# Kernel tuning notes

Hardware: AMD Instinct MI355X
Metric: run time of the kernel (lower is better)

The kernel has to match this reference:

```python
import jax, jax.numpy as jnp
import numpy as np

S, B, H = 512, 32, 1024      # seq, batch, hidden_size
L = 4096                      # total spans (flattened ragged labels)
D = 1024                      # label_size (feature dim)
V = 32000                     # vocab size


def setup_inputs() -> dict:
    key = jax.random.key(0)
    ks = jax.random.split(key, 10)
    hidden = jax.random.normal(ks[0], (S, B, H), dtype=jnp.float32)
    span_bid = jax.random.randint(ks[1], (L,), 0, B)
    span_begin = jax.random.randint(ks[2], (L,), 0, S)
    span_end_m1 = jax.random.randint(ks[3], (L,), 0, S)  # (end - 1) index
    tags = jax.random.randint(ks[4], (L,), 0, V)
    # hidden2feature: Linear(2H -> D) with bias, Tanh
    W1 = jax.random.normal(ks[5], (D, 2 * H), dtype=jnp.float32) * (1.0 / np.sqrt(2 * H))
    b1 = jnp.zeros((D,), dtype=jnp.float32)
    # SoftmaxLoss h2o: Linear(D -> V, bias=False)
    Wout = jax.random.normal(ks[6], (V, D), dtype=jnp.float32) * (1.0 / np.sqrt(D))
    # discard probs from synthetic frequency counts
    counts = jax.random.uniform(ks[7], (V,), minval=1e-5, maxval=1.0)
    freqs = counts / counts.sum()
    discard_probs = jnp.clip(1.0 - jnp.sqrt(1e-4 / freqs), 0.0, None)
    return {"hidden": hidden, "W1": W1, "b1": b1, "Wout": Wout,
            "discard_probs": discard_probs, "span_bid": span_bid,
            "span_begin": span_begin, "span_end_m1": span_end_m1, "tags": tags}


def reference(hidden, W1, b1, Wout, discard_probs, span_bid, span_begin, span_end_m1, tags):
    # gather span endpoint embeddings: [L, H] each
    emb_b = hidden[span_begin, span_bid]
    emb_e = hidden[span_end_m1, span_bid]
    span_emb = jnp.concatenate([emb_b, emb_e], axis=-1)          # [L, 2H]
    feat = jnp.tanh(span_emb @ W1.T + b1)                        # [L, D]
    logits = feat @ Wout.T                                       # [L, V]
    logp = jax.nn.log_softmax(logits, axis=-1)
    nll = -jnp.take_along_axis(logp, tags[:, None], axis=-1)[:, 0]  # [L]
    scaled = 1.0 - discard_probs[tags]
    n_tags = tags.shape[0]
    return jnp.sum(nll * scaled) / (n_tags + 1e-5)
```

## Files before the change

kernel.cpp:

```cpp
#include <hip/hip_runtime.h>
#include <hip/hip_bf16.h>

#define LSPANS 4096
#define BB 32
#define HH 1024
#define DD 1024
#define VV 32000
#define K1 2048
#define NT2 250

typedef unsigned short u16;
typedef __attribute__((ext_vector_type(8))) short bf16x8v;
typedef __attribute__((ext_vector_type(4))) float f32x4v;

__device__ __forceinline__ u16 f2bf(float x) {
  union { float f; unsigned u; } v; v.f = x;
  unsigned r = (v.u >> 16) & 1u;
  return (u16)((v.u + 0x7fffu + r) >> 16);
}

__global__ void cvt_kernel(const float* __restrict__ in, u16* __restrict__ out, int n4) {
  int i = blockIdx.x * blockDim.x + threadIdx.x;
  int stride = gridDim.x * blockDim.x;
  for (; i < n4; i += stride) {
    float4 v = ((const float4*)in)[i];
    ushort4 o;
    o.x = f2bf(v.x); o.y = f2bf(v.y); o.z = f2bf(v.z); o.w = f2bf(v.w);
    ((ushort4*)out)[i] = o;
  }
}

__global__ void gather_kernel(const float* __restrict__ hidden,
                              const int* __restrict__ bid,
                              const int* __restrict__ sb,
                              const int* __restrict__ se,
                              u16* __restrict__ out) {
  int l = blockIdx.x;
  int t = threadIdx.x;
  int b  = bid[l];
  const float* p0 = hidden + ((size_t)sb[l] * BB + b) * HH;
  const float* p1 = hidden + ((size_t)se[l] * BB + b) * HH;
  u16* dst = out + (size_t)l * K1;
  float4 v0 = ((const float4*)p0)[t];
  float4 v1 = ((const float4*)p1)[t];
  ushort4 o0; o0.x = f2bf(v0.x); o0.y = f2bf(v0.y); o0.z = f2bf(v0.z); o0.w = f2bf(v0.w);
  ushort4 o1; o1.x = f2bf(v1.x); o1.y = f2bf(v1.y); o1.z = f2bf(v1.z); o1.w = f2bf(v1.w);
  ((ushort4*)dst)[t]          = o0;
  ((ushort4*)(dst + HH))[t]   = o1;
}

template <int K_, int EPI>
__launch_bounds__(256, 2)
__global__ void gemm_kernel(const u16* __restrict__ A, const u16* __restrict__ B,
                            int Ntot,
                            const float* __restrict__ bias, u16* __restrict__ feat_out,
                            const int* __restrict__ tags,
                            float* __restrict__ pmax, float* __restrict__ psum,
                            float* __restrict__ ltag) {
  __shared__ __align__(16) u16 As[128 * 64];
  __shared__ __align__(16) u16 Bs[128 * 64];
  __shared__ float rmax[2][128];
  __shared__ float rsum[2][128];
  __shared__ int   stags[128];

  const int tid  = threadIdx.x;
  const int lane = tid & 63;
  const int w    = tid >> 6;
  const int wm   = w & 1;
  const int wn   = w >> 1;
  const int q    = lane >> 4;
  const int lm   = lane & 15;
  const int mBase = blockIdx.x * 128;
  const int nBase = blockIdx.y * 128;

  if (EPI == 2 && tid < 128) stags[tid] = tags[mBase + tid];

  f32x4v acc[4][4];
#pragma unroll
  for (int i = 0; i < 4; ++i)
#pragma unroll
    for (int j = 0; j < 4; ++j) acc[i][j] = (f32x4v){0.f, 0.f, 0.f, 0.f};

  const int srow = w * 32 + (lane >> 3);
  const int scol = ((lane & 7) ^ (lane >> 3)) * 8;
  const u16* Ag = A + (size_t)(mBase + srow) * K_ + scol;
  const u16* Bg = B + (size_t)(nBase + srow) * K_ + scol;

  for (int k0 = 0; k0 < K_; k0 += 64) {
#pragma unroll
    for (int c = 0; c < 4; ++c) {
      __builtin_amdgcn_global_load_lds(
          (const __attribute__((address_space(1))) void*)(Ag + k0 + (size_t)c * 8 * K_),
          (__attribute__((address_space(3))) void*)(As + (w * 32 + c * 8) * 64), 16, 0, 0);
    }
#pragma unroll
    for (int c = 0; c < 4; ++c) {
      __builtin_amdgcn_global_load_lds(
          (const __attribute__((address_space(1))) void*)(Bg + k0 + (size_t)c * 8 * K_),
          (__attribute__((address_space(3))) void*)(Bs + (w * 32 + c * 8) * 64), 16, 0, 0);
    }
    __syncthreads();
#pragma unroll
    for (int kk = 0; kk < 64; kk += 32) {
      bf16x8v af[4], bfr[4];
      const int sw = lm & 7;
#pragma unroll
      for (int i = 0; i < 4; ++i) {
        int row = wm * 64 + i * 16 + lm;
        int kch = (kk >> 3) + q;
        af[i] = *(const bf16x8v*)(As + row * 64 + ((kch ^ sw) << 3));
      }
#pragma unroll
      for (int j = 0; j < 4; ++j) {
        int row = wn * 64 + j * 16 + lm;
        int kch = (kk >> 3) + q;
        bfr[j] = *(const bf16x8v*)(Bs + row * 64 + ((kch ^ sw) << 3));
      }
#pragma unroll
      for (int i = 0; i < 4; ++i)
#pragma unroll
        for (int j = 0; j < 4; ++j)
          acc[i][j] = __builtin_amdgcn_mfma_f32_16x16x32_bf16(af[i], bfr[j], acc[i][j], 0, 0, 0);
    }
    __syncthreads();
  }

  if constexpr (EPI == 1) {
    float bj[4];
#pragma unroll
    for (int j = 0; j < 4; ++j) bj[j] = bias[nBase + wn * 64 + j * 16 + lm];
#pragma unroll
    for (int i = 0; i < 4; ++i)
#pragma unroll
      for (int j = 0; j < 4; ++j)
#pragma unroll
        for (int r = 0; r < 4; ++r) {
          int tr = wm * 64 + i * 16 + q * 4 + r;
          int tc = wn * 64 + j * 16 + lm;
          float v = tanhf(acc[i][j][r] + bj[j]);
          feat_out[(size_t)(mBase + tr) * Ntot + nBase + tc] = f2bf(v);
        }
  }

  if constexpr (EPI == 2) {
#pragma unroll
    for (int i = 0; i < 4; ++i)
#pragma unroll
      for (int r = 0; r < 4; ++r) {
        float m = fmaxf(fmaxf(acc[i][0][r], acc[i][1][r]),
                        fmaxf(acc[i][2][r], acc[i][3][r]));
#pragma unroll
        for (int off = 1; off < 16; off <<= 1) m = fmaxf(m, __shfl_xor(m, off, 64));
        if (lm == 0) rmax[wn][wm * 64 + i * 16 + q * 4 + r] = m;
      }
    __syncthreads();
#pragma unroll
    for (int i = 0; i < 4; ++i)
#pragma unroll
      for (int r = 0; r < 4; ++r) {
        int tr = wm * 64 + i * 16 + q * 4 + r;
        float M = fmaxf(rmax[0][tr], rmax[1][tr]);
        float s = __expf(acc[i][0][r] - M) + __expf(acc[i][1][r] - M) +
                  __expf(acc[i][2][r] - M) + __expf(acc[i][3][r] - M);
#pragma unroll
        for (int off = 1; off < 16; off <<= 1) s += __shfl_xor(s, off, 64);
        if (lm == 0) rsum[wn][tr] = s;
      }
    __syncthreads();
    if (tid < 128) {
      float M = fmaxf(rmax[0][tid], rmax[1][tid]);
      float S = rsum[0][tid] + rsum[1][tid];
      pmax[(size_t)blockIdx.y * LSPANS + mBase + tid] = M;
      psum[(size_t)blockIdx.y * LSPANS + mBase + tid] = S;
    }
#pragma unroll
    for (int i = 0; i < 4; ++i)
#pragma unroll
      for (int r = 0; r < 4; ++r) {
        int tr = wm * 64 + i * 16 + q * 4 + r;
        int tg = stags[tr];
#pragma unroll
        for (int j = 0; j < 4; ++j) {
          int gc = nBase + wn * 64 + j * 16 + lm;
          if (tg == gc) ltag[mBase + tr] = acc[i][j][r];
        }
      }
  }
}

__launch_bounds__(256, 2)
__global__ void gemm1n64_kernel(const u16* __restrict__ A, const u16* __restrict__ B,
                                const float* __restrict__ bias,
                                u16* __restrict__ feat_out) {
  __shared__ __align__(16) u16 As[128 * 64];
  __shared__ __align__(16) u16 Bs[64 * 64];

  const int tid  = threadIdx.x;
  const int lane = tid & 63;
  const int w    = tid >> 6;
  const int wm   = w & 1;
  const int wn   = w >> 1;
  const int q    = lane >> 4;
  const int lm   = lane & 15;
  const int mBase = blockIdx.x * 128;
  const int nBase = blockIdx.y * 64;

  f32x4v acc[4][2];
#pragma unroll
  for (int i = 0; i < 4; ++i)
#pragma unroll
    for (int j = 0; j < 2; ++j) acc[i][j] = (f32x4v){0.f, 0.f, 0.f, 0.f};

  const int srowA = w * 32 + (lane >> 3);
  const int srowB = w * 16 + (lane >> 3);
  const int scol  = ((lane & 7) ^ (lane >> 3)) * 8;
  const u16* Ag = A + (size_t)(mBase + srowA) * K1 + scol;
  const u16* Bg = B + (size_t)(nBase + srowB) * K1 + scol;

  for (int k0 = 0; k0 < K1; k0 += 64) {
#pragma unroll
    for (int c = 0; c < 4; ++c) {
      __builtin_amdgcn_global_load_lds(
          (const __attribute__((address_space(1))) void*)(Ag + k0 + (size_t)c * 8 * K1),
          (__attribute__((address_space(3))) void*)(As + (w * 32 + c * 8) * 64), 16, 0, 0);
    }
#pragma unroll
    for (int c = 0; c < 2; ++c) {
      __builtin_amdgcn_global_load_lds(
          (const __attribute__((address_space(1))) void*)(Bg + k0 + (size_t)c * 8 * K1),
          (__attribute__((address_space(3))) void*)(Bs + (w * 16 + c * 8) * 64), 16, 0, 0);
    }
    __syncthreads();
#pragma unroll
    for (int kk = 0; kk < 64; kk += 32) {
      bf16x8v af[4], bfr[2];
      const int sw = lm & 7;
#pragma unroll
      for (int i = 0; i < 4; ++i) {
        int row = wm * 64 + i * 16 + lm;
        int kch = (kk >> 3) + q;
        af[i] = *(const bf16x8v*)(As + row * 64 + ((kch ^ sw) << 3));
      }
#pragma unroll
      for (int j = 0; j < 2; ++j) {
        int row = wn * 32 + j * 16 + lm;
        int kch = (kk >> 3) + q;
        bfr[j] = *(const bf16x8v*)(Bs + row * 64 + ((kch ^ sw) << 3));
      }
#pragma unroll
      for (int i = 0; i < 4; ++i)
#pragma unroll
        for (int j = 0; j < 2; ++j)
          acc[i][j] = __builtin_amdgcn_mfma_f32_16x16x32_bf16(af[i], bfr[j], acc[i][j], 0, 0, 0);
    }
    __syncthreads();
  }

  float bj[2];
#pragma unroll
  for (int j = 0; j < 2; ++j) bj[j] = bias[nBase + wn * 32 + j * 16 + lm];
#pragma unroll
  for (int i = 0; i < 4; ++i)
#pragma unroll
    for (int j = 0; j < 2; ++j)
#pragma unroll
      for (int r = 0; r < 4; ++r) {
        int tr = wm * 64 + i * 16 + q * 4 + r;
        int tc = wn * 32 + j * 16 + lm;
        float v = tanhf(acc[i][j][r] + bj[j]);
        feat_out[(size_t)(mBase + tr) * DD + nBase + tc] = f2bf(v);
      }
}

__global__ void finalize_kernel(const float* __restrict__ pmax, const float* __restrict__ psum,
                                const float* __restrict__ ltag, const int* __restrict__ tags,
                                const float* __restrict__ dprob, float* __restrict__ out) {
  const int lane = threadIdx.x & 63;
  const int wv   = threadIdx.x >> 6;
  const int row  = blockIdx.x * 4 + wv;

  float pmv[4], psv[4];
#pragma unroll
  for (int it = 0; it < 4; ++it) {
    int t = lane + it * 64;
    bool ok = t < NT2;
    pmv[it] = ok ? pmax[(size_t)t * LSPANS + row] : -1e30f;
    psv[it] = ok ? psum[(size_t)t * LSPANS + row] : 0.f;
  }
  float M = fmaxf(fmaxf(pmv[0], pmv[1]), fmaxf(pmv[2], pmv[3]));
#pragma unroll
  for (int off = 1; off < 64; off <<= 1) M = fmaxf(M, __shfl_xor(M, off, 64));
  float s = 0.f;
#pragma unroll
  for (int it = 0; it < 4; ++it) s += psv[it] * __expf(pmv[it] - M);
#pragma unroll
  for (int off = 1; off < 64; off <<= 1) s += __shfl_xor(s, off, 64);

  __shared__ float red[4];
  if (lane == 0) {
    float nll = M + logf(s) - ltag[row];
    float wgt = 1.0f - dprob[tags[row]];
    red[wv] = nll * wgt * (1.0f / (4096.0f + 1e-5f));
  }
  __syncthreads();
  if (threadIdx.x == 0) atomicAdd(out, red[0] + red[1] + red[2] + red[3]);
}

extern "C" void kernel_launch(void* const* d_in, const int* in_sizes, int n_in,
                              void* d_out, int out_size, void* d_ws, size_t ws_size,
                              hipStream_t stream) {
  const float* hidden = (const float*)d_in[0];
  const float* W1     = (const float*)d_in[1];
  const float* b1     = (const float*)d_in[2];
  const float* Wout   = (const float*)d_in[3];
  const float* dprob  = (const float*)d_in[4];
  const int*   bid    = (const int*)d_in[5];
  const int*   sb     = (const int*)d_in[6];
  const int*   se     = (const int*)d_in[7];
  const int*   tags   = (const int*)d_in[8];
  float* out = (float*)d_out;

  char* ws = (char*)d_ws;
  u16* A1    = (u16*)ws;                 ws += (size_t)LSPANS * K1 * 2;
  u16* W1b   = (u16*)ws;                 ws += (size_t)DD * K1 * 2;
  u16* Woutb = (u16*)ws;                 ws += (size_t)VV * DD * 2;
  u16* feat  = (u16*)ws;                 ws += (size_t)LSPANS * DD * 2;
  float* pmax = (float*)ws;              ws += (size_t)NT2 * LSPANS * 4;
  float* psum = (float*)ws;              ws += (size_t)NT2 * LSPANS * 4;
  float* ltag = (float*)ws;              ws += (size_t)LSPANS * 4;

  hipMemsetAsync(d_out, 0, sizeof(float), stream);

  {
    int n4 = DD * K1 / 4;
    cvt_kernel<<<(n4 + 255) / 256, 256, 0, stream>>>(W1, W1b, n4);
  }
  {
    int n4 = VV * DD / 4;
    cvt_kernel<<<(n4 + 255) / 256, 256, 0, stream>>>(Wout, Woutb, n4);
  }
  gather_kernel<<<LSPANS, 256, 0, stream>>>(hidden, bid, sb, se, A1);

  gemm1n64_kernel<<<dim3(LSPANS / 128, DD / 64), 256, 0, stream>>>(
      A1, W1b, b1, feat);

  gemm_kernel<DD, 2><<<dim3(LSPANS / 128, NT2), 256, 0, stream>>>(
      feat, Woutb, VV, nullptr, nullptr, tags, pmax, psum, ltag);

  finalize_kernel<<<LSPANS / 4, 256, 0, stream>>>(pmax, psum, ltag, tags, dprob, out);
}
```

Before: 587.2 us.

## Merge prep kernels and overlap Wout conversion with first GEMM, remap gemm2 tiles

Folds the hidden gather and the W1 conversion into one launch. The Wout fp32-to-bf16 conversion now runs as extra blocks inside the first GEMM launch, so that memory-bound work can overlap with the compute-bound GEMM and launch overhead drops. The second GEMM remaps block indices so consecutive blocks spread across N tiles, which changes L2 reuse of Wout and feat. The cost is more complex heterogeneous blocks, and the conversion blocks may compete with GEMM blocks for CU slots.

After: 611.9 us. +4.2%, slower.

```diff
diff --git a/kernel.cpp b/kernel.cpp
--- a/kernel.cpp
+++ b/kernel.cpp
@@ -19,44 +19,143 @@
   return (u16)((v.u + 0x7fffu + r) >> 16);
 }
 
-__global__ void cvt_kernel(const float* __restrict__ in, u16* __restrict__ out, int n4) {
-  int i = blockIdx.x * blockDim.x + threadIdx.x;
-  int stride = gridDim.x * blockDim.x;
-  for (; i < n4; i += stride) {
-    float4 v = ((const float4*)in)[i];
-    ushort4 o;
-    o.x = f2bf(v.x); o.y = f2bf(v.y); o.z = f2bf(v.z); o.w = f2bf(v.w);
-    ((ushort4*)out)[i] = o;
-  }
-}
-
-__global__ void gather_kernel(const float* __restrict__ hidden,
-                              const int* __restrict__ bid,
-                              const int* __restrict__ sb,
-                              const int* __restrict__ se,
-                              u16* __restrict__ out) {
-  int l = blockIdx.x;
-  int t = threadIdx.x;
-  int b  = bid[l];
-  const float* p0 = hidden + ((size_t)sb[l] * BB + b) * HH;
-  const float* p1 = hidden + ((size_t)se[l] * BB + b) * HH;
-  u16* dst = out + (size_t)l * K1;
-  float4 v0 = ((const float4*)p0)[t];
-  float4 v1 = ((const float4*)p1)[t];
-  ushort4 o0; o0.x = f2bf(v0.x); o0.y = f2bf(v0.y); o0.z = f2bf(v0.z); o0.w = f2bf(v0.w);
-  ushort4 o1; o1.x = f2bf(v1.x); o1.y = f2bf(v1.y); o1.z = f2bf(v1.z); o1.w = f2bf(v1.w);
-  ((ushort4*)dst)[t]          = o0;
-  ((ushort4*)(dst + HH))[t]   = o1;
-}
-
-template <int K_, int EPI>
+__global__ void prep1_kernel(const float* __restrict__ hidden,
+                             const int* __restrict__ bid,
+                             const int* __restrict__ sb,
+                             const int* __restrict__ se,
+                             u16* __restrict__ A1,
+                             const float* __restrict__ W1,
+                             u16* __restrict__ W1b) {
+  const int blk = blockIdx.x;
+  if (blk < LSPANS) {
+    const int l = blk;
+    const int t = threadIdx.x;
+    const int b = bid[l];
+    const float* p0 = hidden + ((size_t)sb[l] * BB + b) * HH;
+    const float* p1 = hidden + ((size_t)se[l] * BB + b) * HH;
+    u16* dst = A1 + (size_t)l * K1;
+    float4 v0 = ((const float4*)p0)[t];
+    float4 v1 = ((const float4*)p1)[t];
+    ushort4 o0; o0.x = f2bf(v0.x); o0.y = f2bf(v0.y); o0.z = f2bf(v0.z); o0.w = f2bf(v0.w);
+    ushort4 o1; o1.x = f2bf(v1.x); o1.y = f2bf(v1.y); o1.z = f2bf(v1.z); o1.w = f2bf(v1.w);
+    ((ushort4*)dst)[t]          = o0;
+    ((ushort4*)(dst + HH))[t]   = o1;
+  } else {
+    const int n4 = DD * K1 / 4;
+    int i = (blk - LSPANS) * 256 + threadIdx.x;
+    const int stride = 512 * 256;
+    for (; i < n4; i += stride) {
+      float4 v = ((const float4*)W1)[i];
+      ushort4 o;
+      o.x = f2bf(v.x); o.y = f2bf(v.y); o.z = f2bf(v.z); o.w = f2bf(v.w);
+      ((ushort4*)W1b)[i] = o;
+    }
+  }
+}
+
 __launch_bounds__(256, 2)
-__global__ void gemm_kernel(const u16* __restrict__ A, const u16* __restrict__ B,
-                            int Ntot,
-                            const float* __restrict__ bias, u16* __restrict__ feat_out,
-                            const int* __restrict__ tags,
-                            float* __restrict__ pmax, float* __restrict__ psum,
-                            float* __restrict__ ltag) {
+__global__ void prep2_kernel(const u16* __restrict__ A, const u16* __restrict__ B,
+                             const float* __restrict__ bias,
+                             u16* __restrict__ feat_out,
+                             const float* __restrict__ Wout,
+                             u16* __restrict__ Woutb) {
+  __shared__ __align__(16) u16 As[128 * 64];
+  __shared__ __align__(16) u16 Bs[64 * 64];
+
+  if (blockIdx.x < 512) {
+    const int tid  = threadIdx.x;
+    const int lane = tid & 63;
+    const int w    = tid >> 6;
+    const int wm   = w & 1;
+    const int wn   = w >> 1;
+    const int q    = lane >> 4;
+    const int lm   = lane & 15;
+    const int mBase = (blockIdx.x & 31) * 128;
+    const int nBase = (blockIdx.x >> 5) * 64;
+
+    f32x4v acc[4][2];
+#pragma unroll
+    for (int i = 0; i < 4; ++i)
+#pragma unroll
+      for (int j = 0; j < 2; ++j) acc[i][j] = (f32x4v){0.f, 0.f, 0.f, 0.f};
+
+    const int srowA = w * 32 + (lane >> 3);
+    const int srowB = w * 16 + (lane >> 3);
+    const int scol  = ((lane & 7) ^ (lane >> 3)) * 8;
+    const u16* Ag = A + (size_t)(mBase + srowA) * K1 + scol;
+    const u16* Bg = B + (size_t)(nBase + srowB) * K1 + scol;
+
+    for (int k0 = 0; k0 < K1; k0 += 64) {
+#pragma unroll
+      for (int c = 0; c < 4; ++c) {
+        __builtin_amdgcn_global_load_lds(
+            (const __attribute__((address_space(1))) void*)(Ag + k0 + (size_t)c * 8 * K1),
+            (__attribute__((address_space(3))) void*)(As + (w * 32 + c * 8) * 64), 16, 0, 0);
+      }
+#pragma unroll
+      for (int c = 0; c < 2; ++c) {
+        __builtin_amdgcn_global_load_lds(
+            (const __attribute__((address_space(1))) void*)(Bg + k0 + (size_t)c * 8 * K1),
+            (__attribute__((address_space(3))) void*)(Bs + (w * 16 + c * 8) * 64), 16, 0, 0);
+      }
+      __syncthreads();
+#pragma unroll
+      for (int kk = 0; kk < 64; kk += 32) {
+        bf16x8v af[4], bfr[2];
+        const int sw = lm & 7;
+#pragma unroll
+        for (int i = 0; i < 4; ++i) {
+          int row = wm * 64 + i * 16 + lm;
+          int kch = (kk >> 3) + q;
+          af[i] = *(const bf16x8v*)(As + row * 64 + ((kch ^ sw) << 3));
+        }
+#pragma unroll
+        for (int j = 0; j < 2; ++j) {
+          int row = wn * 32 + j * 16 + lm;
+          int kch = (kk >> 3) + q;
+          bfr[j] = *(const bf16x8v*)(Bs + row * 64 + ((kch ^ sw) << 3));
+        }
+#pragma unroll
+        for (int i = 0; i < 4; ++i)
+#pragma unroll
+          for (int j = 0; j < 2; ++j)
+            acc[i][j] = __builtin_amdgcn_mfma_f32_16x16x32_bf16(af[i], bfr[j], acc[i][j], 0, 0, 0);
+      }
+      __syncthreads();
+    }
+
+    float bj[2];
+#pragma unroll
+    for (int j = 0; j < 2; ++j) bj[j] = bias[nBase + wn * 32 + j * 16 + lm];
+#pragma unroll
+    for (int i = 0; i < 4; ++i)
+#pragma unroll
+      for (int j = 0; j < 2; ++j)
+#pragma unroll
+        for (int r = 0; r < 4; ++r) {
+          int tr = wm * 64 + i * 16 + q * 4 + r;
+          int tc = wn * 32 + j * 16 + lm;
+          float v = tanhf(acc[i][j][r] + bj[j]);
+          feat_out[(size_t)(mBase + tr) * DD + nBase + tc] = f2bf(v);
+        }
+  } else {
+    const int n4 = VV * DD / 4;
+    int i = (blockIdx.x - 512) * 256 + threadIdx.x;
+    const int stride = 2048 * 256;
+    for (; i < n4; i += stride) {
+      float4 v = ((const float4*)Wout)[i];
+      ushort4 o;
+      o.x = f2bf(v.x); o.y = f2bf(v.y); o.z = f2bf(v.z); o.w = f2bf(v.w);
+      ((ushort4*)Woutb)[i] = o;
+    }
+  }
+}
+
+__launch_bounds__(256, 2)
+__global__ void gemm2_kernel(const u16* __restrict__ A, const u16* __restrict__ B,
+                             const int* __restrict__ tags,
+                             float* __restrict__ pmax, float* __restrict__ psum,
+                             float* __restrict__ ltag) {
   __shared__ __align__(16) u16 As[128 * 64];
   __shared__ __align__(16) u16 Bs[128 * 64];
   __shared__ float rmax[2][128];
@@ -70,10 +169,14 @@
   const int wn   = w >> 1;
   const int q    = lane >> 4;
   const int lm   = lane & 15;
-  const int mBase = blockIdx.x * 128;
-  const int nBase = blockIdx.y * 128;
-
-  if (EPI == 2 && tid < 128) stags[tid] = tags[mBase + tid];
+  const int lin = blockIdx.y * 32 + blockIdx.x;
+  const int nl  = (lin & 7) * 1000 + (lin >> 3);
+  const int bx  = nl & 31;
+  const int by  = nl >> 5;
+  const int mBase = bx * 128;
+  const int nBase = by * 128;
+
+  if (tid < 128) stags[tid] = tags[mBase + tid];
 
   f32x4v acc[4][4];
 #pragma unroll
@@ -83,20 +186,20 @@
 
   const int srow = w * 32 + (lane >> 3);
   const int scol = ((lane & 7) ^ (lane >> 3)) * 8;
-  const u16* Ag = A + (size_t)(mBase + srow) * K_ + scol;
-  const u16* Bg = B + (size_t)(nBase + srow) * K_ + scol;
-
-  for (int k0 = 0; k0 < K_; k0 += 64) {
+  const u16* Ag = A + (size_t)(mBase + srow) * DD + scol;
+  const u16* Bg = B + (size_t)(nBase + srow) * DD + scol;
+
+  for (int k0 = 0; k0 < DD; k0 += 64) {
 #pragma unroll
     for (int c = 0; c < 4; ++c) {
       __builtin_amdgcn_global_load_lds(
-          (const __attribute__((address_space(1))) void*)(Ag + k0 + (size_t)c * 8 * K_),
+          (const __attribute__((address_space(1))) void*)(Ag + k0 + (size_t)c * 8 * DD),
           (__attribute__((address_space(3))) void*)(As + (w * 32 + c * 8) * 64), 16, 0, 0);
     }
 #pragma unroll
     for (int c = 0; c < 4; ++c) {
       __builtin_amdgcn_global_load_lds(
-          (const __attribute__((address_space(1))) void*)(Bg + k0 + (size_t)c * 8 * K_),
+          (const __attribute__((address_space(1))) void*)(Bg + k0 + (size_t)c * 8 * DD),
           (__attribute__((address_space(3))) void*)(Bs + (w * 32 + c * 8) * 64), 16, 0, 0);
     }
     __syncthreads();
@@ -125,151 +228,48 @@
     __syncthreads();
   }
 
-  if constexpr (EPI == 1) {
-    float bj[4];
-#pragma unroll
-    for (int j = 0; j < 4; ++j) bj[j] = bias[nBase + wn * 64 + j * 16 + lm];
-#pragma unroll
-    for (int i = 0; i < 4; ++i)
-#pragma unroll
-      for (int j = 0; j < 4; ++j)
-#pragma unroll
-        for (int r = 0; r < 4; ++r) {
-          int tr = wm * 64 + i * 16 + q * 4 + r;
-          int tc = wn * 64 + j * 16 + lm;
-          float v = tanhf(acc[i][j][r] + bj[j]);
-          feat_out[(size_t)(mBase + tr) * Ntot + nBase + tc] = f2bf(v);
-        }
-  }
-
-  if constexpr (EPI == 2) {
-#pragma unroll
-    for (int i = 0; i < 4; ++i)
-#pragma unroll
-      for (int r = 0; r < 4; ++r) {
-        float m = fmaxf(fmaxf(acc[i][0][r], acc[i][1][r]),
-                        fmaxf(acc[i][2][r], acc[i][3][r]));
-#pragma unroll
-        for (int off = 1; off < 16; off <<= 1) m = fmaxf(m, __shfl_xor(m, off, 64));
-        if (lm == 0) rmax[wn][wm * 64 + i * 16 + q * 4 + r] = m;
-      }
-    __syncthreads();
-#pragma unroll
-    for (int i = 0; i < 4; ++i)
-#pragma unroll
-      for (int r = 0; r < 4; ++r) {
-        int tr = wm * 64 + i * 16 + q * 4 + r;
-        float M = fmaxf(rmax[0][tr], rmax[1][tr]);
-        float s = __expf(acc[i][0][r] - M) + __expf(acc[i][1][r] - M) +
-                  __expf(acc[i][2][r] - M) + __expf(acc[i][3][r] - M);
-#pragma unroll
-        for (int off = 1; off < 16; off <<= 1) s += __shfl_xor(s, off, 64);
-        if (lm == 0) rsum[wn][tr] = s;
-      }
-    __syncthreads();
-    if (tid < 128) {
-      float M = fmaxf(rmax[0][tid], rmax[1][tid]);
-      float S = rsum[0][tid] + rsum[1][tid];
-      pmax[(size_t)blockIdx.y * LSPANS + mBase + tid] = M;
-      psum[(size_t)blockIdx.y * LSPANS + mBase + tid] = S;
-    }
-#pragma unroll
-    for (int i = 0; i < 4; ++i)
-#pragma unroll
-      for (int r = 0; r < 4; ++r) {
-        int tr = wm * 64 + i * 16 + q * 4 + r;
-        int tg = stags[tr];
-#pragma unroll
-        for (int j = 0; j < 4; ++j) {
-          int gc = nBase + wn * 64 + j * 16 + lm;
-          if (tg == gc) ltag[mBase + tr] = acc[i][j][r];
-        }
-      }
-  }
-}
-
-__launch_bounds__(256, 2)
-__global__ void gemm1n64_kernel(const u16* __restrict__ A, const u16* __restrict__ B,
-                                const float* __restrict__ bias,
-                                u16* __restrict__ feat_out) {
-  __shared__ __align__(16) u16 As[128 * 64];
-  __shared__ __align__(16) u16 Bs[64 * 64];
-
-  const int tid  = threadIdx.x;
-  const int lane = tid & 63;
-  const int w    = tid >> 6;
-  const int wm   = w & 1;
-  const int wn   = w >> 1;
-  const int q    = lane >> 4;
-  const int lm   = lane & 15;
-  const int mBase = blockIdx.x * 128;
-  const int nBase = blockIdx.y * 64;
-
-  f32x4v acc[4][2];
 #pragma unroll
   for (int i = 0; i < 4; ++i)
 #pragma unroll
-    for (int j = 0; j < 2; ++j) acc[i][j] = (f32x4v){0.f, 0.f, 0.f, 0.f};
-
-  const int srowA = w * 32 + (lane >> 3);
-  const int srowB = w * 16 + (lane >> 3);
-  const int scol  = ((lane & 7) ^ (lane >> 3)) * 8;
-  const u16* Ag = A + (size_t)(mBase + srowA) * K1 + scol;
-  const u16* Bg = B + (size_t)(nBase + srowB) * K1 + scol;
-
-  for (int k0 = 0; k0 < K1; k0 += 64) {
-#pragma unroll
-    for (int c = 0; c < 4; ++c) {
-      __builtin_amdgcn_global_load_lds(
-          (const __attribute__((address_space(1))) void*)(Ag + k0 + (size_t)c * 8 * K1),
-          (__attribute__((address_space(3))) void*)(As + (w * 32 + c * 8) * 64), 16, 0, 0);
-    }
-#pragma unroll
-    for (int c = 0; c < 2; ++c) {
-      __builtin_amdgcn_global_load_lds(
-          (const __attribute__((address_space(1))) void*)(Bg + k0 + (size_t)c * 8 * K1),
-          (__attribute__((address_space(3))) void*)(Bs + (w * 16 + c * 8) * 64), 16, 0, 0);
-    }
-    __syncthreads();
-#pragma unroll
-    for (int kk = 0; kk < 64; kk += 32) {
-      bf16x8v af[4], bfr[2];
-      const int sw = lm & 7;
-#pragma unroll
-      for (int i = 0; i < 4; ++i) {
-        int row = wm * 64 + i * 16 + lm;
-        int kch = (kk >> 3) + q;
-        af[i] = *(const bf16x8v*)(As + row * 64 + ((kch ^ sw) << 3));
-      }
-#pragma unroll
-      for (int j = 0; j < 2; ++j) {
-        int row = wn * 32 + j * 16 + lm;
-        int kch = (kk >> 3) + q;
-        bfr[j] = *(const bf16x8v*)(Bs + row * 64 + ((kch ^ sw) << 3));
-      }
-#pragma unroll
-      for (int i = 0; i < 4; ++i)
-#pragma unroll
-        for (int j = 0; j < 2; ++j)
-          acc[i][j] = __builtin_amdgcn_mfma_f32_16x16x32_bf16(af[i], bfr[j], acc[i][j], 0, 0, 0);
-    }
-    __syncthreads();
-  }
-
-  float bj[2];
-#pragma unroll
-  for (int j = 0; j < 2; ++j) bj[j] = bias[nBase + wn * 32 + j * 16 + lm];
+    for (int r = 0; r < 4; ++r) {
+      float m = fmaxf(fmaxf(acc[i][0][r], acc[i][1][r]),
+                      fmaxf(acc[i][2][r], acc[i][3][r]));
+#pragma unroll
+      for (int off = 1; off < 16; off <<= 1) m = fmaxf(m, __shfl_xor(m, off, 64));
+      if (lm == 0) rmax[wn][wm * 64 + i * 16 + q * 4 + r] = m;
+    }
+  __syncthreads();
 #pragma unroll
   for (int i = 0; i < 4; ++i)
 #pragma unroll
-    for (int j = 0; j < 2; ++j)
-#pragma unroll
-      for (int r = 0; r < 4; ++r) {
-        int tr = wm * 64 + i * 16 + q * 4 + r;
-        int tc = wn * 32 + j * 16 + lm;
-        float v = tanhf(acc[i][j][r] + bj[j]);
-        feat_out[(size_t)(mBase + tr) * DD + nBase + tc] = f2bf(v);
-      }
+    for (int r = 0; r < 4; ++r) {
+      int tr = wm * 64 + i * 16 + q * 4 + r;
+      float M = fmaxf(rmax[0][tr], rmax[1][tr]);
+      float s = __expf(acc[i][0][r] - M) + __expf(acc[i][1][r] - M) +
+                __expf(acc[i][2][r] - M) + __expf(acc[i][3][r] - M);
+#pragma unroll
+      for (int off = 1; off < 16; off <<= 1) s += __shfl_xor(s, off, 64);
+      if (lm == 0) rsum[wn][tr] = s;
+    }
+  __syncthreads();
+  if (tid < 128) {
+    float M = fmaxf(rmax[0][tid], rmax[1][tid]);
+    float S = rsum[0][tid] + rsum[1][tid];
+    pmax[(size_t)by * LSPANS + mBase + tid] = M;
+    psum[(size_t)by * LSPANS + mBase + tid] = S;
+  }
+#pragma unroll
+  for (int i = 0; i < 4; ++i)
+#pragma unroll
+    for (int r = 0; r < 4; ++r) {
+      int tr = wm * 64 + i * 16 + q * 4 + r;
+      int tg = stags[tr];
+#pragma unroll
+      for (int j = 0; j < 4; ++j) {
+        int gc = nBase + wn * 64 + j * 16 + lm;
+        if (tg == gc) ltag[mBase + tr] = acc[i][j][r];
+      }
+    }
 }
 
 __global__ void finalize_kernel(const float* __restrict__ pmax, const float* __restrict__ psum,
@@ -331,21 +331,12 @@
 
   hipMemsetAsync(d_out, 0, sizeof(float), stream);
 
-  {
-    int n4 = DD * K1 / 4;
-    cvt_kernel<<<(n4 + 255) / 256, 256, 0, stream>>>(W1, W1b, n4);
-  }
-  {
-    int n4 = VV * DD / 4;
-    cvt_kernel<<<(n4 + 255) / 256, 256, 0, stream>>>(Wout, Woutb, n4);
-  }
-  gather_kernel<<<LSPANS, 256, 0, stream>>>(hidden, bid, sb, se, A1);
-
-  gemm1n64_kernel<<<dim3(LSPANS / 128, DD / 64), 256, 0, stream>>>(
-      A1, W1b, b1, feat);
-
-  gemm_kernel<DD, 2><<<dim3(LSPANS / 128, NT2), 256, 0, stream>>>(
-      feat, Woutb, VV, nullptr, nullptr, tags, pmax, psum, ltag);
+  prep1_kernel<<<LSPANS + 512, 256, 0, stream>>>(hidden, bid, sb, se, A1, W1, W1b);
+
+  prep2_kernel<<<512 + 2048, 256, 0, stream>>>(A1, W1b, b1, feat, Wout, Woutb);
+
+  gemm2_kernel<<<dim3(32, NT2), 256, 0, stream>>>(
+      feat, Woutb, tags, pmax, psum, ltag);
 
   finalize_kernel<<<LSPANS / 4, 256, 0, stream>>>(pmax, psum, ltag, tags, dprob, out);
 }
```
